# Kernel tuning notes

Hardware: AMD Instinct MI355X
Metric: run time of the kernel (lower is better)

## Reference

```python
import jax, jax.numpy as jnp
import numpy as np

DIAG_FLOOR = 0.1
DIAG_CEIL = 1.0


def setup_inputs() -> dict:
    key = jax.random.key(0)
    k1, k2, k3, k4 = jax.random.split(key, 4)
    m, in_f, out_f = 16384, 1024, 2048
    z = jax.random.normal(k1, (m, in_f), dtype=jnp.float32)
    diag_params = jax.random.normal(k2, (out_f, in_f), dtype=jnp.float32)
    mean_params = 5.0 * jax.random.normal(k3, (out_f, in_f, 1), dtype=jnp.float32)
    scale_params = jax.random.normal(k4, (out_f,), dtype=jnp.float32)
    return {"z": z, "diag_params": diag_params, "mean_params": mean_params,
            "scale_params": scale_params}


def reference(z, diag_params, mean_params, scale_params):
    # Clamp diag to (0.1, 1.0) via sigmoid; clamp scale via tanh.
    d = DIAG_FLOOR + (DIAG_CEIL - DIAG_FLOOR) * jax.nn.sigmoid(diag_params)  # (out, in)
    mean = mean_params[..., 0]  # (out, in)

    # Diagonal covariance => quadratic forms reduce to elementwise products:
    # z_cov_z[m,k]    = sum_i d[k,i] * z[m,i]^2
    # mean_cov_mean[k]= sum_i d[k,i] * mean[k,i]^2
    # z_cov_mean[m,k] = sum_i z[m,i] * d[k,i] * mean[k,i]
    z_cov_z = jnp.einsum('mi,ki->mk', z * z, d)          # (m, out)
    mean_cov_mean = jnp.sum(d * mean * mean, axis=1)      # (out,)
    z_cov_mean = jnp.einsum('mi,ki->mk', z, d * mean)     # (m, out)

    scaling = jnp.tanh(scale_params)                      # (out,)
    return scaling * jnp.exp(-z_cov_z - mean_cov_mean + 2.0 * z_cov_mean)
```

## Files before the change

kernel.cpp:

```cpp
#include <hip/hip_runtime.h>
#include <hip/hip_bf16.h>
#include <cstdint>
#include <cstddef>

#define M_DIM 16384
#define IN_F  1024
#define OUT_F 2048
#define K_CAT 2048
#define NT    (K_CAT / 32)

typedef float f32x4 __attribute__((ext_vector_type(4)));
typedef short short8 __attribute__((ext_vector_type(8)));

__device__ __forceinline__ void gld_lds16(const void* gptr, void* lptr) {
    __builtin_amdgcn_global_load_lds(
        (const __attribute__((address_space(1))) uint32_t*)gptr,
        (__attribute__((address_space(3))) uint32_t*)lptr,
        16 , 0 , 0 );
}

__global__ __launch_bounds__(256) void prep_z_kernel(const float* __restrict__ z,
                                                     __hip_bfloat16* __restrict__ A) {
    const int idx = blockIdx.x * 256 + threadIdx.x;
    const int m  = idx >> 7;
    const int c8 = (idx & 127) * 8;
    const float4 v0 = ((const float4*)z)[idx * 2];
    const float4 v1 = ((const float4*)z)[idx * 2 + 1];
    const float x[8] = {v0.x, v0.y, v0.z, v0.w, v1.x, v1.y, v1.z, v1.w};
    __hip_bfloat16 q[8], r[8];
#pragma unroll
    for (int j = 0; j < 8; ++j) {
        q[j] = __float2bfloat16(x[j] * x[j]);
        r[j] = __float2bfloat16(x[j]);
    }
    __hip_bfloat16* rowp = A + (size_t)m * K_CAT;
    *(uint4*)&rowp[c8]        = *(uint4*)q;
    *(uint4*)&rowp[IN_F + c8] = *(uint4*)r;
}

__global__ __launch_bounds__(256) void prep_b_kernel(const float* __restrict__ diag,
                                                     const float* __restrict__ mean,
                                                     const float* __restrict__ scale,
                                                     __hip_bfloat16* __restrict__ B,
                                                     float* __restrict__ mcm,
                                                     float* __restrict__ ts) {
    const int k = blockIdx.x;
    const int t = threadIdx.x;
    const float4 dp = ((const float4*)(diag + (size_t)k * IN_F))[t];
    const float4 mp = ((const float4*)(mean + (size_t)k * IN_F))[t];
    const float dx[4] = {dp.x, dp.y, dp.z, dp.w};
    const float mx[4] = {mp.x, mp.y, mp.z, mp.w};
    __hip_bfloat16 nb[4], pb[4];
    float acc = 0.f;
#pragma unroll
    for (int j = 0; j < 4; ++j) {
        const float d = 0.1f + 0.9f / (1.f + __expf(-dx[j]));
        nb[j] = __float2bfloat16(-d);
        pb[j] = __float2bfloat16(2.f * d * mx[j]);
        acc += d * mx[j] * mx[j];
    }
    __hip_bfloat16* rowp = B + (size_t)k * K_CAT;
    *(uint2*)&rowp[t * 4]        = *(uint2*)nb;
    *(uint2*)&rowp[IN_F + t * 4] = *(uint2*)pb;
#pragma unroll
    for (int off = 32; off > 0; off >>= 1) acc += __shfl_down(acc, off);
    __shared__ float red[4];
    if ((t & 63) == 0) red[t >> 6] = acc;
    __syncthreads();
    if (t == 0) {
        mcm[k] = red[0] + red[1] + red[2] + red[3];
        ts[k]  = tanhf(scale[k]);
    }
}

__global__ __launch_bounds__(512, 2) void gemm_exp_kernel(
    const __hip_bfloat16* __restrict__ A,
    const __hip_bfloat16* __restrict__ B,
    const float* __restrict__ mcm,
    const float* __restrict__ ts,
    float* __restrict__ out) {
    __shared__ __align__(16) __hip_bfloat16 smem[4][2][8192];

    const int t = threadIdx.x;
    const int wg = ((blockIdx.x & 7) << 6) | (blockIdx.x >> 3);
    const int tn = wg & 7;
    const int tm = wg >> 3;

    const int c0 = t, c1 = t + 512;
    const int r0 = c0 >> 2, s0 = c0 & 3;
    const int r1 = c1 >> 2, s1 = c1 & 3;
    const __hip_bfloat16* gA0 = A + (size_t)(tm * 256 + r0) * K_CAT + s0 * 8;
    const __hip_bfloat16* gA1 = A + (size_t)(tm * 256 + r1) * K_CAT + s1 * 8;
    const __hip_bfloat16* gB0 = B + (size_t)(tn * 256 + r0) * K_CAT + s0 * 8;
    const __hip_bfloat16* gB1 = B + (size_t)(tn * 256 + r1) * K_CAT + s1 * 8;

#define ISSUE_A(buf_, kt_) do { \
        gld_lds16(gA0 + (kt_) * 32, &smem[buf_][0][c0 * 8]); \
        gld_lds16(gA1 + (kt_) * 32, &smem[buf_][0][c1 * 8]); } while (0)
#define ISSUE_B(buf_, kt_) do { \
        gld_lds16(gB0 + (kt_) * 32, &smem[buf_][1][c0 * 8]); \
        gld_lds16(gB1 + (kt_) * 32, &smem[buf_][1][c1 * 8]); } while (0)

    const int wid = t >> 6, lane = t & 63;
    const int wmb = (wid >> 2) * 128;
    const int wnb = (wid & 3) * 64;
    const int l15 = lane & 15, l4 = lane >> 4;
    int offA[8], offB[4];
#pragma unroll
    for (int fm = 0; fm < 8; ++fm) offA[fm] = (wmb + fm * 16 + l15) * 32 + l4 * 8;
#pragma unroll
    for (int fn = 0; fn < 4; ++fn) offB[fn] = (wnb + fn * 16 + l15) * 32 + l4 * 8;

    f32x4 acc[8][4] = {};

    ISSUE_A(0, 0); ISSUE_B(0, 0);
    ISSUE_A(1, 1); ISSUE_B(1, 1);
    ISSUE_A(2, 2); ISSUE_B(2, 2);
    asm volatile("s_waitcnt vmcnt(8)" ::: "memory");
    __builtin_amdgcn_s_barrier();
    __builtin_amdgcn_sched_barrier(0);

#pragma unroll 4
    for (int kt = 0; kt < NT; ++kt) {
        const int buf  = kt & 3;
        const int pf   = (kt < NT - 3) ? kt + 3 : NT - 1;
        const int pbuf = (kt + 3) & 3;

        short8 bfr[4], af0[4];
#pragma unroll
        for (int fn = 0; fn < 4; ++fn) bfr[fn] = *(const short8*)&smem[buf][1][offB[fn]];
#pragma unroll
        for (int fm = 0; fm < 4; ++fm) af0[fm] = *(const short8*)&smem[buf][0][offA[fm]];
        ISSUE_A(pbuf, pf);
        __builtin_amdgcn_sched_barrier(0);
        __builtin_amdgcn_s_barrier();
        asm volatile("s_waitcnt lgkmcnt(0)" ::: "memory");
        __builtin_amdgcn_sched_barrier(0);
        __builtin_amdgcn_s_setprio(1);
#pragma unroll
        for (int fm = 0; fm < 4; ++fm)
#pragma unroll
            for (int fn = 0; fn < 4; ++fn)
                acc[fm][fn] = __builtin_amdgcn_mfma_f32_16x16x32_bf16(
                    af0[fm], bfr[fn], acc[fm][fn], 0, 0, 0);
        __builtin_amdgcn_s_setprio(0);
        __builtin_amdgcn_sched_barrier(0);
        __builtin_amdgcn_s_barrier();

        short8 af1[4];
#pragma unroll
        for (int fm = 0; fm < 4; ++fm) af1[fm] = *(const short8*)&smem[buf][0][offA[fm + 4]];
        ISSUE_B(pbuf, pf);
        __builtin_amdgcn_sched_barrier(0);
        __builtin_amdgcn_s_barrier();
        asm volatile("s_waitcnt lgkmcnt(0)" ::: "memory");
        __builtin_amdgcn_sched_barrier(0);
        __builtin_amdgcn_s_setprio(1);
#pragma unroll
        for (int fm = 0; fm < 4; ++fm)
#pragma unroll
            for (int fn = 0; fn < 4; ++fn)
                acc[fm + 4][fn] = __builtin_amdgcn_mfma_f32_16x16x32_bf16(
                    af1[fm], bfr[fn], acc[fm + 4][fn], 0, 0, 0);
        __builtin_amdgcn_s_setprio(0);
        __builtin_amdgcn_sched_barrier(0);
        asm volatile("s_waitcnt vmcnt(8)" ::: "memory");
        __builtin_amdgcn_s_barrier();
        __builtin_amdgcn_sched_barrier(0);
    }
#undef ISSUE_A
#undef ISSUE_B

#pragma unroll
    for (int fn = 0; fn < 4; ++fn) {
        const int gn = tn * 256 + wnb + fn * 16 + l15;
        const float tsv = ts[gn];
        const float mv  = mcm[gn];
#pragma unroll
        for (int fm = 0; fm < 8; ++fm) {
            const int gm0 = tm * 256 + wmb + fm * 16 + l4 * 4;
#pragma unroll
            for (int r = 0; r < 4; ++r)
                out[(size_t)(gm0 + r) * OUT_F + gn] = tsv * __expf(acc[fm][fn][r] - mv);
        }
    }
}

extern "C" void kernel_launch(void* const* d_in, const int* in_sizes, int n_in,
                              void* d_out, int out_size, void* d_ws, size_t ws_size,
                              hipStream_t stream) {
    const float* z     = (const float*)d_in[0];
    const float* diag  = (const float*)d_in[1];
    const float* mean  = (const float*)d_in[2];
    const float* scale = (const float*)d_in[3];
    float* out = (float*)d_out;

    char* ws = (char*)d_ws;
    const size_t A_BYTES = (size_t)M_DIM * K_CAT * sizeof(__hip_bfloat16);
    const size_t B_BYTES = (size_t)OUT_F * K_CAT * sizeof(__hip_bfloat16);
    __hip_bfloat16* Abuf = (__hip_bfloat16*)ws;
    __hip_bfloat16* Bbuf = (__hip_bfloat16*)(ws + A_BYTES);
    float* mcm = (float*)(ws + A_BYTES + B_BYTES);
    float* ts  = (float*)(ws + A_BYTES + B_BYTES + 8192);

    prep_z_kernel<<<(M_DIM * IN_F / 8) / 256, 256, 0, stream>>>(z, Abuf);
    prep_b_kernel<<<OUT_F, 256, 0, stream>>>(diag, mean, scale, Bbuf, mcm, ts);
    gemm_exp_kernel<<<(M_DIM / 256) * (OUT_F / 256), 512, 0, stream>>>(
        Abuf, Bbuf, mcm, ts, out);
}
```

Measured before the change: 324.2 us.

## XOR-swizzle LDS tile layout and merge k-step into single MFMA phase

```diff
diff --git a/kernel.cpp b/kernel.cpp
--- a/kernel.cpp
+++ b/kernel.cpp
@@ -87,8 +87,10 @@
     const int tm = wg >> 3;
 
     const int c0 = t, c1 = t + 512;
-    const int r0 = c0 >> 2, s0 = c0 & 3;
-    const int r1 = c1 >> 2, s1 = c1 & 3;
+    const int r0 = c0 >> 2, u0 = c0 & 3;
+    const int r1 = c1 >> 2, u1 = c1 & 3;
+    const int s0 = u0 ^ ((r0 >> 1) & 3);
+    const int s1 = u1 ^ ((r1 >> 1) & 3);
     const __hip_bfloat16* gA0 = A + (size_t)(tm * 256 + r0) * K_CAT + s0 * 8;
     const __hip_bfloat16* gA1 = A + (size_t)(tm * 256 + r1) * K_CAT + s1 * 8;
     const __hip_bfloat16* gB0 = B + (size_t)(tn * 256 + r0) * K_CAT + s0 * 8;
@@ -107,9 +109,15 @@
     const int l15 = lane & 15, l4 = lane >> 4;
     int offA[8], offB[4];
 #pragma unroll
-    for (int fm = 0; fm < 8; ++fm) offA[fm] = (wmb + fm * 16 + l15) * 32 + l4 * 8;
+    for (int fm = 0; fm < 8; ++fm) {
+        const int r = wmb + fm * 16 + l15;
+        offA[fm] = r * 32 + (l4 ^ ((r >> 1) & 3)) * 8;
+    }
 #pragma unroll
-    for (int fn = 0; fn < 4; ++fn) offB[fn] = (wnb + fn * 16 + l15) * 32 + l4 * 8;
+    for (int fn = 0; fn < 4; ++fn) {
+        const int r = wnb + fn * 16 + l15;
+        offB[fn] = r * 32 + (l4 ^ ((r >> 1) & 3)) * 8;
+    }
 
     f32x4 acc[8][4] = {};
 
@@ -126,42 +134,23 @@
         const int pf   = (kt < NT - 3) ? kt + 3 : NT - 1;
         const int pbuf = (kt + 3) & 3;
 
-        short8 bfr[4], af0[4];
+        short8 bfr[4], af[8];
 #pragma unroll
         for (int fn = 0; fn < 4; ++fn) bfr[fn] = *(const short8*)&smem[buf][1][offB[fn]];
 #pragma unroll
-        for (int fm = 0; fm < 4; ++fm) af0[fm] = *(const short8*)&smem[buf][0][offA[fm]];
+        for (int fm = 0; fm < 8; ++fm) af[fm]  = *(const short8*)&smem[buf][0][offA[fm]];
         ISSUE_A(pbuf, pf);
+        ISSUE_B(pbuf, pf);
         __builtin_amdgcn_sched_barrier(0);
-        __builtin_amdgcn_s_barrier();
         asm volatile("s_waitcnt lgkmcnt(0)" ::: "memory");
         __builtin_amdgcn_sched_barrier(0);
         __builtin_amdgcn_s_setprio(1);
 #pragma unroll
-        for (int fm = 0; fm < 4; ++fm)
+        for (int fm = 0; fm < 8; ++fm)
 #pragma unroll
             for (int fn = 0; fn < 4; ++fn)
                 acc[fm][fn] = __builtin_amdgcn_mfma_f32_16x16x32_bf16(
-                    af0[fm], bfr[fn], acc[fm][fn], 0, 0, 0);
-        __builtin_amdgcn_s_setprio(0);
-        __builtin_amdgcn_sched_barrier(0);
-        __builtin_amdgcn_s_barrier();
-
-        short8 af1[4];
-#pragma unroll
-        for (int fm = 0; fm < 4; ++fm) af1[fm] = *(const short8*)&smem[buf][0][offA[fm + 4]];
-        ISSUE_B(pbuf, pf);
-        __builtin_amdgcn_sched_barrier(0);
-        __builtin_amdgcn_s_barrier();
-        asm volatile("s_waitcnt lgkmcnt(0)" ::: "memory");
-        __builtin_amdgcn_sched_barrier(0);
-        __builtin_amdgcn_s_setprio(1);
-#pragma unroll
-        for (int fm = 0; fm < 4; ++fm)
-#pragma unroll
-            for (int fn = 0; fn < 4; ++fn)
-                acc[fm + 4][fn] = __builtin_amdgcn_mfma_f32_16x16x32_bf16(
-                    af1[fm], bfr[fn], acc[fm + 4][fn], 0, 0, 0);
+                    af[fm], bfr[fn], acc[fm][fn], 0, 0, 0);
         __builtin_amdgcn_s_setprio(0);
         __builtin_amdgcn_sched_barrier(0);
         asm volatile("s_waitcnt vmcnt(8)" ::: "memory");
```

Result: faster. 315.7 us (-2.6%).
